# Performance work log

Hardware: AMD Instinct MI355X
Metric: run time of the kernel (lower is better)

Reference implementation:

```python
import jax, jax.numpy as jnp
import numpy as np

BN_EPS = 1e-5

def setup_inputs() -> dict:
    key = jax.random.key(0)
    ks = jax.random.split(key, 16)
    B, N = 64, 1024
    dims = [3, 64, 128, 256]
    H = 256
    inp = {"x": jax.random.normal(ks[0], (B, dims[0], N), dtype=jnp.float32)}
    for i in range(3):
        ci, co = dims[i], dims[i + 1]
        inp[f"w{i+1}"] = jax.random.normal(ks[1 + i], (co, ci), dtype=jnp.float32) * (1.0 / np.sqrt(ci))
        inp[f"b{i+1}"] = jnp.zeros((co,), dtype=jnp.float32)
        inp[f"g{i+1}"] = jnp.ones((co,), dtype=jnp.float32)
        inp[f"be{i+1}"] = jnp.zeros((co,), dtype=jnp.float32)
    inp["A"] = jnp.eye(H, dtype=jnp.float32) + 0.01 * jax.random.normal(ks[10], (H, H), dtype=jnp.float32)
    inp["Bm"] = 0.01 * jax.random.normal(ks[11], (H, dims[-1]), dtype=jnp.float32)
    inp["Cm"] = 0.01 * jax.random.normal(ks[12], (dims[-1], H), dtype=jnp.float32)
    return inp


def _conv_bn_relu(h, w, b, g, be):
    # h: [B, Cin, N]; 1x1 conv == channel matmul
    y = jnp.einsum('oi,bin->bon', w, h) + b[None, :, None]
    mu = jnp.mean(y, axis=(0, 2), keepdims=True)
    var = jnp.var(y, axis=(0, 2), keepdims=True)
    y = (y - mu) * jax.lax.rsqrt(var + BN_EPS)
    y = y * g[None, :, None] + be[None, :, None]
    return jax.nn.relu(y)


def reference(x, w1, b1, g1, be1, w2, b2, g2, be2, w3, b3, g3, be3, A, Bm, Cm):
    h = _conv_bn_relu(x, w1, b1, g1, be1)
    h = _conv_bn_relu(h, w2, b2, g2, be2)
    h = _conv_bn_relu(h, w3, b3, g3, be3)
    u = jnp.transpose(h, (0, 2, 1))  # [B, N, C]
    Bsz = u.shape[0]
    H = A.shape[0]
    A_norm = A / (jnp.linalg.norm(A, ord=2) + 1e-5)
    uB = u @ Bm.T  # precompute input projection: [B, N, H]

    def step(hstate, ut):
        hstate = jax.nn.relu(hstate @ A_norm.T + ut)
        return hstate, hstate @ Cm.T

    h0 = jnp.zeros((Bsz, H), dtype=x.dtype)
    _, ys = jax.lax.scan(step, h0, jnp.transpose(uB, (1, 0, 2)))  # ys: [N, B, Cout]
    y = jnp.transpose(ys, (1, 2, 0))  # [B, Cout, N]
    return y
```

## Files before the change

kernel.cpp:

```cpp
#include <hip/hip_runtime.h>

#define B_SZ 64
#define N_SZ 1024
#define C1   64
#define C2   128
#define C3   256
#define H_SZ 256

__global__ void k_btb(const float* __restrict__ A, float* __restrict__ B0) {
  int i = blockIdx.x;
  int j = threadIdx.x;
  float acc = 0.f;
  for (int k = 0; k < 256; ++k)
    acc = fmaf(A[k * 256 + i], A[k * 256 + j], acc);
  B0[i * 256 + j] = acc;
}

__global__ void k_bsq(const float* __restrict__ Bin, float* __restrict__ Bout) {
  __shared__ float diag[256];
  int i = blockIdx.x, j = threadIdx.x;
  diag[j] = Bin[j * 256 + j];
  __syncthreads();
  float tr = 0.f;
  for (int k = 0; k < 256; ++k) tr += diag[k];
  float inv = 1.0f / tr;
  float acc = 0.f;
  for (int k = 0; k < 256; ++k)
    acc = fmaf(Bin[i * 256 + k], Bin[k * 256 + j], acc);
  Bout[i * 256 + j] = acc * inv * inv;
}

__global__ void k_sfin(const float* __restrict__ Bf, const float* __restrict__ B0,
                       float* __restrict__ sinv) {
  __shared__ float v[256], w[256];
  __shared__ float red[256];
  __shared__ int redi[256];
  int t = threadIdx.x;
  red[t] = Bf[t * 256 + t];
  redi[t] = t;
  __syncthreads();
  for (int s = 128; s > 0; s >>= 1) {
    if (t < s) {
      if (red[t + s] > red[t]) { red[t] = red[t + s]; redi[t] = redi[t + s]; }
    }
    __syncthreads();
  }
  int jmax = redi[0];
  __syncthreads();
  v[t] = Bf[t * 256 + jmax];
  __syncthreads();
  float acc = 0.f;
  for (int k = 0; k < 256; ++k) acc = fmaf(B0[t * 256 + k], v[k], acc);
  w[t] = acc;
  __syncthreads();
  red[t] = v[t] * w[t];
  __syncthreads();
  for (int s = 128; s > 0; s >>= 1) { if (t < s) red[t] += red[t + s]; __syncthreads(); }
  float num = red[0];
  __syncthreads();
  red[t] = v[t] * v[t];
  __syncthreads();
  for (int s = 128; s > 0; s >>= 1) { if (t < s) red[t] += red[t + s]; __syncthreads(); }
  if (t == 0) {
    float lam = num / red[0];
    float sg = sqrtf(lam);
    *sinv = 1.0f / (sg + 1e-5f);
  }
}

__global__ void k_conv1(const float* __restrict__ x, const float* __restrict__ w,
                        const float* __restrict__ bias, float* __restrict__ y) {
  int b = blockIdx.x >> 2;
  int n = ((blockIdx.x & 3) << 8) + threadIdx.x;
  const float* xb = x + (size_t)b * 3 * N_SZ;
  float x0 = xb[n], x1 = xb[N_SZ + n], x2 = xb[2 * N_SZ + n];
  float* yb = y + (size_t)b * C1 * N_SZ;
#pragma unroll 4
  for (int o = 0; o < C1; ++o) {
    float r = fmaf(w[o * 3 + 0], x0,
              fmaf(w[o * 3 + 1], x1,
              fmaf(w[o * 3 + 2], x2, bias[o])));
    yb[(size_t)o * N_SZ + n] = r;
  }
}

__global__ void k_stats(const float* __restrict__ y, int C,
                        const float* __restrict__ g, const float* __restrict__ be,
                        float* __restrict__ coef) {
  int c = blockIdx.x;
  int t = threadIdx.x;
  float s1 = 0.f, s2 = 0.f;
  for (int b = 0; b < B_SZ; ++b) {
    const float4* p = (const float4*)(y + ((size_t)b * C + c) * N_SZ);
    float4 v = p[t];
    s1 += v.x + v.y + v.z + v.w;
    s2 += v.x * v.x + v.y * v.y + v.z * v.z + v.w * v.w;
  }
  __shared__ float r1[256], r2[256];
  r1[t] = s1; r2[t] = s2;
  __syncthreads();
  for (int s = 128; s > 0; s >>= 1) {
    if (t < s) { r1[t] += r1[t + s]; r2[t] += r2[t + s]; }
    __syncthreads();
  }
  if (t == 0) {
    const float M = (float)(B_SZ * N_SZ);
    float mu = r1[0] / M;
    float var = r2[0] / M - mu * mu;
    float sc = g[c] * rsqrtf(var + 1e-5f);
    coef[c] = sc;
    coef[C + c] = be[c] - mu * sc;
  }
}


#define GEMM_COMPUTE8(ATc, BTc)                                      \
  _Pragma("unroll") for (int kk = 0; kk < 8; ++kk) {                 \
    float av[2][4], bv[2][4];                                        \
    *(float4*)av[0] = *(const float4*)&ATc[kk][ty * 4];              \
    *(float4*)av[1] = *(const float4*)&ATc[kk][64 + ty * 4];         \
    *(float4*)bv[0] = *(const float4*)&BTc[kk][tx * 4];              \
    *(float4*)bv[1] = *(const float4*)&BTc[kk][64 + tx * 4];         \
    _Pragma("unroll") for (int p = 0; p < 2; ++p)                    \
      _Pragma("unroll") for (int q = 0; q < 2; ++q)                  \
        _Pragma("unroll") for (int i = 0; i < 4; ++i)                \
          _Pragma("unroll") for (int j = 0; j < 4; ++j)              \
            acc[p][q][i][j] = fmaf(av[p][i], bv[q][j], acc[p][q][i][j]); \
  }

#define RAW_BARRIER()                                    \
  asm volatile("s_waitcnt lgkmcnt(0)" ::: "memory");     \
  __builtin_amdgcn_s_barrier();                          \
  asm volatile("" ::: "memory");

template <int K, int CO>
__global__ __launch_bounds__(256, 2) void k_convG(
    const float* __restrict__ hin, const float* __restrict__ coef,
    const float* __restrict__ w, const float* __restrict__ bias,
    float* __restrict__ y) {
  __shared__ float At[2][8][132];
  __shared__ float Bt[2][8][132];
  const int n0 = blockIdx.x * 128, o0 = blockIdx.y * 128, b = blockIdx.z;
  const int t = threadIdx.x, tx = t & 15, ty = t >> 4;
  const int wo = t & 127, wk = (t >> 7) * 4;
  const int hr = t >> 5, hc = (t & 31) * 4;
  const float* hb = hin + (size_t)b * K * N_SZ + n0;
  float acc[2][2][4][4] = {};
  float4 wreg = *(const float4*)(w + (size_t)(o0 + wo) * K + wk);
  float4 hreg = *(const float4*)(hb + (size_t)hr * N_SZ + hc);
  float scR = coef[hr], shR = coef[K + hr];
  At[0][wk + 0][wo] = wreg.x; At[0][wk + 1][wo] = wreg.y;
  At[0][wk + 2][wo] = wreg.z; At[0][wk + 3][wo] = wreg.w;
  {
    float4 u;
    u.x = fmaxf(fmaf(hreg.x, scR, shR), 0.f);
    u.y = fmaxf(fmaf(hreg.y, scR, shR), 0.f);
    u.z = fmaxf(fmaf(hreg.z, scR, shR), 0.f);
    u.w = fmaxf(fmaf(hreg.w, scR, shR), 0.f);
    *(float4*)&Bt[0][hr][hc] = u;
  }
  __syncthreads();
  constexpr int NT = K / 8;
  for (int kt = 0; kt < NT; ++kt) {
    const int cur = kt & 1;
    if (kt + 1 < NT) {
      const int k0 = (kt + 1) * 8;
      wreg = *(const float4*)(w + (size_t)(o0 + wo) * K + k0 + wk);
      hreg = *(const float4*)(hb + (size_t)(k0 + hr) * N_SZ + hc);
      scR = coef[k0 + hr]; shR = coef[K + k0 + hr];
    }
    GEMM_COMPUTE8(At[cur], Bt[cur]);
    if (kt + 1 < NT) {
      const int nx = cur ^ 1;
      At[nx][wk + 0][wo] = wreg.x; At[nx][wk + 1][wo] = wreg.y;
      At[nx][wk + 2][wo] = wreg.z; At[nx][wk + 3][wo] = wreg.w;
      float4 u;
      u.x = fmaxf(fmaf(hreg.x, scR, shR), 0.f);
      u.y = fmaxf(fmaf(hreg.y, scR, shR), 0.f);
      u.z = fmaxf(fmaf(hreg.z, scR, shR), 0.f);
      u.w = fmaxf(fmaf(hreg.w, scR, shR), 0.f);
      *(float4*)&Bt[nx][hr][hc] = u;
      RAW_BARRIER();
    }
  }
#pragma unroll
  for (int p = 0; p < 2; ++p)
#pragma unroll
    for (int i = 0; i < 4; ++i) {
      const int row = o0 + p * 64 + ty * 4 + i;
      const float bvv = bias[row];
      float* yr = y + ((size_t)b * CO + row) * N_SZ + n0;
      float4 v0 = {acc[p][0][i][0] + bvv, acc[p][0][i][1] + bvv,
                   acc[p][0][i][2] + bvv, acc[p][0][i][3] + bvv};
      float4 v1 = {acc[p][1][i][0] + bvv, acc[p][1][i][1] + bvv,
                   acc[p][1][i][2] + bvv, acc[p][1][i][3] + bvv};
      *(float4*)(yr + tx * 4) = v0;
      *(float4*)(yr + 64 + tx * 4) = v1;
    }
}

__global__ __launch_bounds__(256, 2) void k_uBG(
    const float* __restrict__ y3, const float* __restrict__ coef,
    const float* __restrict__ Bm, float* __restrict__ uB) {
  __shared__ float Xt[2][8][132];
  __shared__ float Bt[2][8][132];
  const int n0 = blockIdx.x * 128, h0 = blockIdx.y * 128, b = blockIdx.z;
  const int t = threadIdx.x, tx = t & 15, ty = t >> 4;
  const int xr = t >> 5, xc = (t & 31) * 4;
  const int bh = t & 127, bk = (t >> 7) * 4;
  const float* yb = y3 + (size_t)b * C3 * N_SZ + n0;
  float acc[2][2][4][4] = {};
  float4 xreg = *(const float4*)(yb + (size_t)xr * N_SZ + xc);
  float scR = coef[xr], shR = coef[C3 + xr];
  float4 breg = *(const float4*)(Bm + (size_t)(h0 + bh) * C3 + bk);
  {
    float4 u;
    u.x = fmaxf(fmaf(xreg.x, scR, shR), 0.f);
    u.y = fmaxf(fmaf(xreg.y, scR, shR), 0.f);
    u.z = fmaxf(fmaf(xreg.z, scR, shR), 0.f);
    u.w = fmaxf(fmaf(xreg.w, scR, shR), 0.f);
    *(float4*)&Xt[0][xr][xc] = u;
    Bt[0][bk + 0][bh] = breg.x; Bt[0][bk + 1][bh] = breg.y;
    Bt[0][bk + 2][bh] = breg.z; Bt[0][bk + 3][bh] = breg.w;
  }
  __syncthreads();
  constexpr int NT = C3 / 8;
  for (int kt = 0; kt < NT; ++kt) {
    const int cur = kt & 1;
    if (kt + 1 < NT) {
      const int c0 = (kt + 1) * 8;
      xreg = *(const float4*)(yb + (size_t)(c0 + xr) * N_SZ + xc);
      scR = coef[c0 + xr]; shR = coef[C3 + c0 + xr];
      breg = *(const float4*)(Bm + (size_t)(h0 + bh) * C3 + c0 + bk);
    }
    GEMM_COMPUTE8(Xt[cur], Bt[cur]);
    if (kt + 1 < NT) {
      const int nx = cur ^ 1;
      float4 u;
      u.x = fmaxf(fmaf(xreg.x, scR, shR), 0.f);
      u.y = fmaxf(fmaf(xreg.y, scR, shR), 0.f);
      u.z = fmaxf(fmaf(xreg.z, scR, shR), 0.f);
      u.w = fmaxf(fmaf(xreg.w, scR, shR), 0.f);
      *(float4*)&Xt[nx][xr][xc] = u;
      Bt[nx][bk + 0][bh] = breg.x; Bt[nx][bk + 1][bh] = breg.y;
      Bt[nx][bk + 2][bh] = breg.z; Bt[nx][bk + 3][bh] = breg.w;
      RAW_BARRIER();
    }
  }
#pragma unroll
  for (int p = 0; p < 2; ++p)
#pragma unroll
    for (int i = 0; i < 4; ++i) {
      const int nrow = n0 + p * 64 + ty * 4 + i;
      float* orow = uB + ((size_t)b * N_SZ + nrow) * H_SZ + h0;
      *(float4*)(orow + tx * 4) = *(float4*)acc[p][0][i];
      *(float4*)(orow + 64 + tx * 4) = *(float4*)acc[p][1][i];
    }
}

__global__ __launch_bounds__(256, 2) void k_ymmG(
    const float* __restrict__ hs, const float* __restrict__ Cm,
    float* __restrict__ y) {
  __shared__ float Ct[2][8][132];
  __shared__ float Ht[2][8][132];
  const int n0 = blockIdx.x * 128, co0 = blockIdx.y * 128, b = blockIdx.z;
  const int t = threadIdx.x, tx = t & 15, ty = t >> 4;
  const int cc = t & 127, ck = (t >> 7) * 4;
  const float* hbase = hs + ((size_t)b * N_SZ + n0) * H_SZ;
  float acc[2][2][4][4] = {};
  float4 creg = *(const float4*)(Cm + (size_t)(co0 + cc) * H_SZ + ck);
  float4 hreg = *(const float4*)(hbase + (size_t)cc * H_SZ + ck);
  Ct[0][ck + 0][cc] = creg.x; Ct[0][ck + 1][cc] = creg.y;
  Ct[0][ck + 2][cc] = creg.z; Ct[0][ck + 3][cc] = creg.w;
  Ht[0][ck + 0][cc] = hreg.x; Ht[0][ck + 1][cc] = hreg.y;
  Ht[0][ck + 2][cc] = hreg.z; Ht[0][ck + 3][cc] = hreg.w;
  __syncthreads();
  constexpr int NT = H_SZ / 8;
  for (int kt = 0; kt < NT; ++kt) {
    const int cur = kt & 1;
    if (kt + 1 < NT) {
      const int h0 = (kt + 1) * 8;
      creg = *(const float4*)(Cm + (size_t)(co0 + cc) * H_SZ + h0 + ck);
      hreg = *(const float4*)(hbase + (size_t)cc * H_SZ + h0 + ck);
    }
    GEMM_COMPUTE8(Ct[cur], Ht[cur]);
    if (kt + 1 < NT) {
      const int nx = cur ^ 1;
      Ct[nx][ck + 0][cc] = creg.x; Ct[nx][ck + 1][cc] = creg.y;
      Ct[nx][ck + 2][cc] = creg.z; Ct[nx][ck + 3][cc] = creg.w;
      Ht[nx][ck + 0][cc] = hreg.x; Ht[nx][ck + 1][cc] = hreg.y;
      Ht[nx][ck + 2][cc] = hreg.z; Ht[nx][ck + 3][cc] = hreg.w;
      RAW_BARRIER();
    }
  }
#pragma unroll
  for (int p = 0; p < 2; ++p)
#pragma unroll
    for (int i = 0; i < 4; ++i) {
      const int row = co0 + p * 64 + ty * 4 + i;
      float* yr = y + ((size_t)b * C3 + row) * N_SZ + n0;
      *(float4*)(yr + tx * 4) = *(float4*)acc[p][0][i];
      *(float4*)(yr + 64 + tx * 4) = *(float4*)acc[p][1][i];
    }
}

__device__ __forceinline__ float dpp_xor1(float x) {
  int i = __builtin_amdgcn_update_dpp(0, __float_as_int(x), 0xB1, 0xF, 0xF, true);
  return __int_as_float(i);
}

__global__ __launch_bounds__(512, 1) void k_scan(
    const float* __restrict__ A, const float* __restrict__ sinvp,
    const float* __restrict__ uB, float* __restrict__ hs) {
  __shared__ float h_lds[256];
  __shared__ float part[2][8][256];
  const int b = blockIdx.x;
  const int t = threadIdx.x;
  const int lane = t & 63;
  const int wv = t >> 6;
  const float sinv = *sinvp;
  float a0[32], a1[32], a2[32], a3[32];
  {
    const float* r0 = A + (size_t)(lane) * 256 + wv * 32;
    const float* r1 = A + (size_t)(lane + 64) * 256 + wv * 32;
    const float* r2 = A + (size_t)(lane + 128) * 256 + wv * 32;
    const float* r3 = A + (size_t)(lane + 192) * 256 + wv * 32;
#pragma unroll
    for (int j = 0; j < 32; ++j) {
      a0[j] = r0[j] * sinv; a1[j] = r1[j] * sinv;
      a2[j] = r2[j] * sinv; a3[j] = r3[j] * sinv;
    }
  }
  if (t < 256) h_lds[t] = 0.f;
  __syncthreads();
  const int i_r = wv * 32 + (lane >> 1);
  const int c0 = (lane & 1) * 4;
  const float* ub = uB + (size_t)b * N_SZ * H_SZ;
  float* ho = hs + (size_t)b * N_SZ * H_SZ;
  float u_cur = ub[i_r];
  for (int s = 0; s < N_SZ; ++s) {
    float u_next = 0.f;
    if (s + 1 < N_SZ) u_next = ub[(size_t)(s + 1) * H_SZ + i_r];
    const float4* hp = (const float4*)(h_lds + wv * 32);
    float acc0 = 0.f, acc1 = 0.f, acc2 = 0.f, acc3 = 0.f;
#pragma unroll
    for (int q = 0; q < 8; ++q) {
      const float4 h4 = hp[q];
      acc0 = fmaf(a0[q * 4 + 0], h4.x, acc0);
      acc0 = fmaf(a0[q * 4 + 1], h4.y, acc0);
      acc0 = fmaf(a0[q * 4 + 2], h4.z, acc0);
      acc0 = fmaf(a0[q * 4 + 3], h4.w, acc0);
      acc1 = fmaf(a1[q * 4 + 0], h4.x, acc1);
      acc1 = fmaf(a1[q * 4 + 1], h4.y, acc1);
      acc1 = fmaf(a1[q * 4 + 2], h4.z, acc1);
      acc1 = fmaf(a1[q * 4 + 3], h4.w, acc1);
      acc2 = fmaf(a2[q * 4 + 0], h4.x, acc2);
      acc2 = fmaf(a2[q * 4 + 1], h4.y, acc2);
      acc2 = fmaf(a2[q * 4 + 2], h4.z, acc2);
      acc2 = fmaf(a2[q * 4 + 3], h4.w, acc2);
      acc3 = fmaf(a3[q * 4 + 0], h4.x, acc3);
      acc3 = fmaf(a3[q * 4 + 1], h4.y, acc3);
      acc3 = fmaf(a3[q * 4 + 2], h4.z, acc3);
      acc3 = fmaf(a3[q * 4 + 3], h4.w, acc3);
    }
    const int buf = s & 1;
    part[buf][wv][lane] = acc0;
    part[buf][wv][lane + 64] = acc1;
    part[buf][wv][lane + 128] = acc2;
    part[buf][wv][lane + 192] = acc3;
    asm volatile("s_waitcnt lgkmcnt(0)" ::: "memory");
    __builtin_amdgcn_s_barrier();
    asm volatile("" ::: "memory");
    float s0 = part[buf][c0 + 0][i_r];
    float s1 = part[buf][c0 + 1][i_r];
    float s2 = part[buf][c0 + 2][i_r];
    float s3 = part[buf][c0 + 3][i_r];
    float sum = (s0 + s1) + (s2 + s3);
    sum += dpp_xor1(sum);
    float pv = fmaxf(sum + u_cur, 0.f);
    h_lds[i_r] = pv;
    if ((lane & 1) == 0) ho[(size_t)s * H_SZ + i_r] = pv;
    u_cur = u_next;
    asm volatile("s_waitcnt lgkmcnt(0)" ::: "memory");
  }
}

extern "C" void kernel_launch(void* const* d_in, const int* in_sizes, int n_in,
                              void* d_out, int out_size, void* d_ws, size_t ws_size,
                              hipStream_t stream) {
  const float* x   = (const float*)d_in[0];
  const float* w1  = (const float*)d_in[1];
  const float* b1  = (const float*)d_in[2];
  const float* g1  = (const float*)d_in[3];
  const float* be1 = (const float*)d_in[4];
  const float* w2  = (const float*)d_in[5];
  const float* b2  = (const float*)d_in[6];
  const float* g2  = (const float*)d_in[7];
  const float* be2 = (const float*)d_in[8];
  const float* w3  = (const float*)d_in[9];
  const float* b3  = (const float*)d_in[10];
  const float* g3  = (const float*)d_in[11];
  const float* be3 = (const float*)d_in[12];
  const float* A   = (const float*)d_in[13];
  const float* Bm  = (const float*)d_in[14];
  const float* Cm  = (const float*)d_in[15];
  float* out = (float*)d_out;

  char* ws = (char*)d_ws;
  const size_t MB = 1024ull * 1024ull;
  float* y1 = (float*)(ws + 0);
  float* y2 = (float*)(ws + 16 * MB);
  float* y3 = (float*)(ws + 48 * MB);
  float* hs = (float*)(ws + 0);
  char* sp = ws + 112 * MB;
  float* B0 = (float*)(sp);
  float* P  = (float*)(sp + 256 * 1024);
  float* Q  = (float*)(sp + 512 * 1024);
  float* sinv  = (float*)(sp + 768 * 1024);
  float* coef1 = (float*)(sp + 768 * 1024 + 1024);
  float* coef2 = (float*)(sp + 768 * 1024 + 4096);
  float* coef3 = (float*)(sp + 768 * 1024 + 8192);

  k_btb<<<256, 256, 0, stream>>>(A, B0);
  {
    float* bufs[2] = {P, Q};
    const float* cur = B0;
    for (int it = 0; it < 12; ++it) {
      float* nxt = bufs[it & 1];
      k_bsq<<<256, 256, 0, stream>>>(cur, nxt);
      cur = nxt;
    }
    k_sfin<<<1, 256, 0, stream>>>(cur, B0, sinv);
  }

  k_conv1<<<dim3(B_SZ * 4), 256, 0, stream>>>(x, w1, b1, y1);
  k_stats<<<C1, 256, 0, stream>>>(y1, C1, g1, be1, coef1);
  k_convG<C1, C2><<<dim3(8, 1, B_SZ), 256, 0, stream>>>(y1, coef1, w2, b2, y2);
  k_stats<<<C2, 256, 0, stream>>>(y2, C2, g2, be2, coef2);
  k_convG<C2, C3><<<dim3(8, 2, B_SZ), 256, 0, stream>>>(y2, coef2, w3, b3, y3);
  k_stats<<<C3, 256, 0, stream>>>(y3, C3, g3, be3, coef3);

  k_uBG<<<dim3(8, 2, B_SZ), 256, 0, stream>>>(y3, coef3, Bm, out);

  k_scan<<<dim3(B_SZ), 512, 0, stream>>>(A, sinv, out, hs);

  k_ymmG<<<dim3(8, 2, B_SZ), 256, 0, stream>>>(hs, Cm, out);
}
```

Measured before the change: 1.109 ms.

## Process two batch sequences per scan block to amortize barriers and latency

The recurrent scan kernel now handles two independent batch elements per workgroup, interleaving their mat-vecs and sharing one barrier per timestep, and launches half as many blocks. This is meant to hide LDS and barrier latency in the serial recurrence with independent work, since each step is latency-bound. In exchange each block does twice the FMA work per step and only 32 blocks run, leaving many compute units idle on a large GPU.

```diff
diff --git a/kernel.cpp b/kernel.cpp
--- a/kernel.cpp
+++ b/kernel.cpp
@@ -309,11 +309,33 @@
   return __int_as_float(i);
 }
 
+#define SCAN_MATVEC(HP, O0, O1, O2, O3)                  \
+  _Pragma("unroll") for (int q = 0; q < 8; ++q) {        \
+    const float4 h4 = HP[q];                             \
+    O0 = fmaf(a0[q * 4 + 0], h4.x, O0);                  \
+    O0 = fmaf(a0[q * 4 + 1], h4.y, O0);                  \
+    O0 = fmaf(a0[q * 4 + 2], h4.z, O0);                  \
+    O0 = fmaf(a0[q * 4 + 3], h4.w, O0);                  \
+    O1 = fmaf(a1[q * 4 + 0], h4.x, O1);                  \
+    O1 = fmaf(a1[q * 4 + 1], h4.y, O1);                  \
+    O1 = fmaf(a1[q * 4 + 2], h4.z, O1);                  \
+    O1 = fmaf(a1[q * 4 + 3], h4.w, O1);                  \
+    O2 = fmaf(a2[q * 4 + 0], h4.x, O2);                  \
+    O2 = fmaf(a2[q * 4 + 1], h4.y, O2);                  \
+    O2 = fmaf(a2[q * 4 + 2], h4.z, O2);                  \
+    O2 = fmaf(a2[q * 4 + 3], h4.w, O2);                  \
+    O3 = fmaf(a3[q * 4 + 0], h4.x, O3);                  \
+    O3 = fmaf(a3[q * 4 + 1], h4.y, O3);                  \
+    O3 = fmaf(a3[q * 4 + 2], h4.z, O3);                  \
+    O3 = fmaf(a3[q * 4 + 3], h4.w, O3);                  \
+  }
+
 __global__ __launch_bounds__(512, 1) void k_scan(
     const float* __restrict__ A, const float* __restrict__ sinvp,
     const float* __restrict__ uB, float* __restrict__ hs) {
-  __shared__ float h_lds[256];
-  __shared__ float part[2][8][256];
+  __shared__ float h0_lds[256], h1_lds[256];
+  __shared__ float part0[2][8][256];
+  __shared__ float part1[2][8][256];
   const int b = blockIdx.x;
   const int t = threadIdx.x;
   const int lane = t & 63;
@@ -331,56 +353,66 @@
       a2[j] = r2[j] * sinv; a3[j] = r3[j] * sinv;
     }
   }
-  if (t < 256) h_lds[t] = 0.f;
+  if (t < 256) { h0_lds[t] = 0.f; h1_lds[t] = 0.f; }
   __syncthreads();
   const int i_r = wv * 32 + (lane >> 1);
   const int c0 = (lane & 1) * 4;
-  const float* ub = uB + (size_t)b * N_SZ * H_SZ;
-  float* ho = hs + (size_t)b * N_SZ * H_SZ;
-  float u_cur = ub[i_r];
+  const float* ub0 = uB + (size_t)b * N_SZ * H_SZ;
+  const float* ub1 = uB + (size_t)(b + 32) * N_SZ * H_SZ;
+  float* ho0 = hs + (size_t)b * N_SZ * H_SZ;
+  float* ho1 = hs + (size_t)(b + 32) * N_SZ * H_SZ;
+  float u0 = ub0[i_r], u1 = ub1[i_r];
   for (int s = 0; s < N_SZ; ++s) {
-    float u_next = 0.f;
-    if (s + 1 < N_SZ) u_next = ub[(size_t)(s + 1) * H_SZ + i_r];
-    const float4* hp = (const float4*)(h_lds + wv * 32);
-    float acc0 = 0.f, acc1 = 0.f, acc2 = 0.f, acc3 = 0.f;
-#pragma unroll
-    for (int q = 0; q < 8; ++q) {
-      const float4 h4 = hp[q];
-      acc0 = fmaf(a0[q * 4 + 0], h4.x, acc0);
-      acc0 = fmaf(a0[q * 4 + 1], h4.y, acc0);
-      acc0 = fmaf(a0[q * 4 + 2], h4.z, acc0);
-      acc0 = fmaf(a0[q * 4 + 3], h4.w, acc0);
-      acc1 = fmaf(a1[q * 4 + 0], h4.x, acc1);
-      acc1 = fmaf(a1[q * 4 + 1], h4.y, acc1);
-      acc1 = fmaf(a1[q * 4 + 2], h4.z, acc1);
-      acc1 = fmaf(a1[q * 4 + 3], h4.w, acc1);
-      acc2 = fmaf(a2[q * 4 + 0], h4.x, acc2);
-      acc2 = fmaf(a2[q * 4 + 1], h4.y, acc2);
-      acc2 = fmaf(a2[q * 4 + 2], h4.z, acc2);
-      acc2 = fmaf(a2[q * 4 + 3], h4.w, acc2);
-      acc3 = fmaf(a3[q * 4 + 0], h4.x, acc3);
-      acc3 = fmaf(a3[q * 4 + 1], h4.y, acc3);
-      acc3 = fmaf(a3[q * 4 + 2], h4.z, acc3);
-      acc3 = fmaf(a3[q * 4 + 3], h4.w, acc3);
+    float un0 = 0.f, un1 = 0.f;
+    if (s + 1 < N_SZ) {
+      un0 = ub0[(size_t)(s + 1) * H_SZ + i_r];
+      un1 = ub1[(size_t)(s + 1) * H_SZ + i_r];
     }
     const int buf = s & 1;
-    part[buf][wv][lane] = acc0;
-    part[buf][wv][lane + 64] = acc1;
-    part[buf][wv][lane + 128] = acc2;
-    part[buf][wv][lane + 192] = acc3;
+    const float4* hp0 = (const float4*)(h0_lds + wv * 32);
+    const float4* hp1 = (const float4*)(h1_lds + wv * 32);
+    {
+      float p0 = 0.f, p1 = 0.f, p2 = 0.f, p3 = 0.f;
+      SCAN_MATVEC(hp0, p0, p1, p2, p3);
+      part0[buf][wv][lane] = p0;
+      part0[buf][wv][lane + 64] = p1;
+      part0[buf][wv][lane + 128] = p2;
+      part0[buf][wv][lane + 192] = p3;
+    }
+    {
+      float p0 = 0.f, p1 = 0.f, p2 = 0.f, p3 = 0.f;
+      SCAN_MATVEC(hp1, p0, p1, p2, p3);
+      part1[buf][wv][lane] = p0;
+      part1[buf][wv][lane + 64] = p1;
+      part1[buf][wv][lane + 128] = p2;
+      part1[buf][wv][lane + 192] = p3;
+    }
     asm volatile("s_waitcnt lgkmcnt(0)" ::: "memory");
     __builtin_amdgcn_s_barrier();
     asm volatile("" ::: "memory");
-    float s0 = part[buf][c0 + 0][i_r];
-    float s1 = part[buf][c0 + 1][i_r];
-    float s2 = part[buf][c0 + 2][i_r];
-    float s3 = part[buf][c0 + 3][i_r];
-    float sum = (s0 + s1) + (s2 + s3);
-    sum += dpp_xor1(sum);
-    float pv = fmaxf(sum + u_cur, 0.f);
-    h_lds[i_r] = pv;
-    if ((lane & 1) == 0) ho[(size_t)s * H_SZ + i_r] = pv;
-    u_cur = u_next;
+    {
+      float s0 = part0[buf][c0 + 0][i_r];
+      float s1 = part0[buf][c0 + 1][i_r];
+      float s2 = part0[buf][c0 + 2][i_r];
+      float s3 = part0[buf][c0 + 3][i_r];
+      float t0 = part1[buf][c0 + 0][i_r];
+      float t1 = part1[buf][c0 + 1][i_r];
+      float t2 = part1[buf][c0 + 2][i_r];
+      float t3 = part1[buf][c0 + 3][i_r];
+      float sum0 = (s0 + s1) + (s2 + s3);
+      float sum1 = (t0 + t1) + (t2 + t3);
+      sum0 += dpp_xor1(sum0);
+      sum1 += dpp_xor1(sum1);
+      float pv0 = fmaxf(sum0 + u0, 0.f);
+      float pv1 = fmaxf(sum1 + u1, 0.f);
+      h0_lds[i_r] = pv0;
+      h1_lds[i_r] = pv1;
+      if ((lane & 1) == 0) {
+        ho0[(size_t)s * H_SZ + i_r] = pv0;
+        ho1[(size_t)s * H_SZ + i_r] = pv1;
+      }
+    }
+    u0 = un0; u1 = un1;
     asm volatile("s_waitcnt lgkmcnt(0)" ::: "memory");
   }
 }
@@ -442,7 +474,7 @@
 
   k_uBG<<<dim3(8, 2, B_SZ), 256, 0, stream>>>(y3, coef3, Bm, out);
 
-  k_scan<<<dim3(B_SZ), 512, 0, stream>>>(A, sinv, out, hs);
+  k_scan<<<dim3(B_SZ / 2), 512, 0, stream>>>(A, sinv, out, hs);
 
   k_ymmG<<<dim3(8, 2, B_SZ), 256, 0, stream>>>(hs, Cm, out);
 }
```

Measured after the change: 1.530 ms. 37.9% more time.

## Rework scan reduction to single-buffered two-barrier scheme and raise GEMM occupancy hint

Applied to the files above, without the earlier changes.

The scan kernel drops the double-buffered partial-sum array and the DPP pair reduction. Instead, 256 threads each sum all 8 wave partials for one hidden unit, and a second barrier per step protects the single buffer. This removes the shuffle step and the split work, but adds a barrier on the serial critical path and leaves half the threads idle during the reduction. Separately, the launch-bounds occupancy hint for the three tiled GEMM kernels goes from 2 to 3 blocks per SIMD, which may cap registers.

```diff
diff --git a/kernel.cpp b/kernel.cpp
--- a/kernel.cpp
+++ b/kernel.cpp
@@ -134,7 +134,7 @@
   asm volatile("" ::: "memory");
 
 template <int K, int CO>
-__global__ __launch_bounds__(256, 2) void k_convG(
+__global__ __launch_bounds__(256, 3) void k_convG(
     const float* __restrict__ hin, const float* __restrict__ coef,
     const float* __restrict__ w, const float* __restrict__ bias,
     float* __restrict__ y) {
@@ -199,7 +199,7 @@
     }
 }
 
-__global__ __launch_bounds__(256, 2) void k_uBG(
+__global__ __launch_bounds__(256, 3) void k_uBG(
     const float* __restrict__ y3, const float* __restrict__ coef,
     const float* __restrict__ Bm, float* __restrict__ uB) {
   __shared__ float Xt[2][8][132];
@@ -258,7 +258,7 @@
     }
 }
 
-__global__ __launch_bounds__(256, 2) void k_ymmG(
+__global__ __launch_bounds__(256, 3) void k_ymmG(
     const float* __restrict__ hs, const float* __restrict__ Cm,
     float* __restrict__ y) {
   __shared__ float Ct[2][8][132];
@@ -304,84 +304,61 @@
     }
 }
 
-__device__ __forceinline__ float dpp_xor1(float x) {
-  int i = __builtin_amdgcn_update_dpp(0, __float_as_int(x), 0xB1, 0xF, 0xF, true);
-  return __int_as_float(i);
-}
-
 __global__ __launch_bounds__(512, 1) void k_scan(
     const float* __restrict__ A, const float* __restrict__ sinvp,
     const float* __restrict__ uB, float* __restrict__ hs) {
   __shared__ float h_lds[256];
-  __shared__ float part[2][8][256];
+  __shared__ float part[8][256];
   const int b = blockIdx.x;
   const int t = threadIdx.x;
   const int lane = t & 63;
   const int wv = t >> 6;
   const float sinv = *sinvp;
-  float a0[32], a1[32], a2[32], a3[32];
-  {
-    const float* r0 = A + (size_t)(lane) * 256 + wv * 32;
-    const float* r1 = A + (size_t)(lane + 64) * 256 + wv * 32;
-    const float* r2 = A + (size_t)(lane + 128) * 256 + wv * 32;
-    const float* r3 = A + (size_t)(lane + 192) * 256 + wv * 32;
-#pragma unroll
-    for (int j = 0; j < 32; ++j) {
-      a0[j] = r0[j] * sinv; a1[j] = r1[j] * sinv;
-      a2[j] = r2[j] * sinv; a3[j] = r3[j] * sinv;
-    }
+  float areg[4][32];
+#pragma unroll
+  for (int k = 0; k < 4; ++k) {
+    const float* r = A + (size_t)(lane + 64 * k) * 256 + wv * 32;
+#pragma unroll
+    for (int j = 0; j < 32; ++j) areg[k][j] = r[j] * sinv;
   }
   if (t < 256) h_lds[t] = 0.f;
   __syncthreads();
-  const int i_r = wv * 32 + (lane >> 1);
-  const int c0 = (lane & 1) * 4;
   const float* ub = uB + (size_t)b * N_SZ * H_SZ;
   float* ho = hs + (size_t)b * N_SZ * H_SZ;
-  float u_cur = ub[i_r];
+  float u_cur = (t < 256) ? ub[t] : 0.f;
   for (int s = 0; s < N_SZ; ++s) {
     float u_next = 0.f;
-    if (s + 1 < N_SZ) u_next = ub[(size_t)(s + 1) * H_SZ + i_r];
-    const float4* hp = (const float4*)(h_lds + wv * 32);
-    float acc0 = 0.f, acc1 = 0.f, acc2 = 0.f, acc3 = 0.f;
+    if (t < 256 && s + 1 < N_SZ) u_next = ub[(size_t)(s + 1) * H_SZ + t];
+    const float4* hp = ((const float4*)h_lds) + wv * 8;
+    float acc[4] = {0.f, 0.f, 0.f, 0.f};
 #pragma unroll
     for (int q = 0; q < 8; ++q) {
       const float4 h4 = hp[q];
-      acc0 = fmaf(a0[q * 4 + 0], h4.x, acc0);
-      acc0 = fmaf(a0[q * 4 + 1], h4.y, acc0);
-      acc0 = fmaf(a0[q * 4 + 2], h4.z, acc0);
-      acc0 = fmaf(a0[q * 4 + 3], h4.w, acc0);
-      acc1 = fmaf(a1[q * 4 + 0], h4.x, acc1);
-      acc1 = fmaf(a1[q * 4 + 1], h4.y, acc1);
-      acc1 = fmaf(a1[q * 4 + 2], h4.z, acc1);
-      acc1 = fmaf(a1[q * 4 + 3], h4.w, acc1);
-      acc2 = fmaf(a2[q * 4 + 0], h4.x, acc2);
-      acc2 = fmaf(a2[q * 4 + 1], h4.y, acc2);
-      acc2 = fmaf(a2[q * 4 + 2], h4.z, acc2);
-      acc2 = fmaf(a2[q * 4 + 3], h4.w, acc2);
-      acc3 = fmaf(a3[q * 4 + 0], h4.x, acc3);
-      acc3 = fmaf(a3[q * 4 + 1], h4.y, acc3);
-      acc3 = fmaf(a3[q * 4 + 2], h4.z, acc3);
-      acc3 = fmaf(a3[q * 4 + 3], h4.w, acc3);
-    }
-    const int buf = s & 1;
-    part[buf][wv][lane] = acc0;
-    part[buf][wv][lane + 64] = acc1;
-    part[buf][wv][lane + 128] = acc2;
-    part[buf][wv][lane + 192] = acc3;
+#pragma unroll
+      for (int k = 0; k < 4; ++k) {
+        acc[k] = fmaf(areg[k][q * 4 + 0], h4.x, acc[k]);
+        acc[k] = fmaf(areg[k][q * 4 + 1], h4.y, acc[k]);
+        acc[k] = fmaf(areg[k][q * 4 + 2], h4.z, acc[k]);
+        acc[k] = fmaf(areg[k][q * 4 + 3], h4.w, acc[k]);
+      }
+    }
+    part[wv][lane] = acc[0];
+    part[wv][lane + 64] = acc[1];
+    part[wv][lane + 128] = acc[2];
+    part[wv][lane + 192] = acc[3];
     asm volatile("s_waitcnt lgkmcnt(0)" ::: "memory");
     __builtin_amdgcn_s_barrier();
-    asm volatile("" ::: "memory");
-    float s0 = part[buf][c0 + 0][i_r];
-    float s1 = part[buf][c0 + 1][i_r];
-    float s2 = part[buf][c0 + 2][i_r];
-    float s3 = part[buf][c0 + 3][i_r];
-    float sum = (s0 + s1) + (s2 + s3);
-    sum += dpp_xor1(sum);
-    float pv = fmaxf(sum + u_cur, 0.f);
-    h_lds[i_r] = pv;
-    if ((lane & 1) == 0) ho[(size_t)s * H_SZ + i_r] = pv;
+    if (t < 256) {
+      float p = u_cur;
+#pragma unroll
+      for (int c = 0; c < 8; ++c) p += part[c][t];
+      p = fmaxf(p, 0.f);
+      h_lds[t] = p;
+      ho[(size_t)s * H_SZ + t] = p;
+    }
     u_cur = u_next;
     asm volatile("s_waitcnt lgkmcnt(0)" ::: "memory");
+    __builtin_amdgcn_s_barrier();
   }
 }
 
```

After: 1.123 ms. Within noise of the previous version (+1.3%).
